# Kernel tuning notes

Hardware: AMD Instinct MI355X
Metric: run time of the kernel (lower is better)

Reference implementation:

```python
import jax, jax.numpy as jnp
import numpy as np

N = 100000   # nodes
E = 400000   # edges per relation
D = 256      # in_dim == out_dim
H = 8        # heads
DK = D // H  # 32
R = 2        # relations
SQRT_DK = float(np.sqrt(DK))


def setup_inputs() -> dict:
    key = jax.random.key(0)
    ks = jax.random.split(key, 16)
    s = 1.0 / np.sqrt(D)
    h = jax.random.normal(ks[0], (N, D), jnp.float32)
    src0 = jax.random.randint(ks[1], (E,), 0, N, jnp.int32)
    dst0 = jax.random.randint(ks[2], (E,), 0, N, jnp.int32)
    src1 = jax.random.randint(ks[3], (E,), 0, N, jnp.int32)
    dst1 = jax.random.randint(ks[4], (E,), 0, N, jnp.int32)
    Wk = jax.random.normal(ks[5], (D, D), jnp.float32) * s
    Wq = jax.random.normal(ks[6], (D, D), jnp.float32) * s
    Wv = jax.random.normal(ks[7], (D, D), jnp.float32) * s
    Wa = jax.random.normal(ks[8], (D, D), jnp.float32) * s
    bk = jnp.zeros((D,), jnp.float32)
    bq = jnp.zeros((D,), jnp.float32)
    bv = jnp.zeros((D,), jnp.float32)
    ba = jnp.zeros((D,), jnp.float32)
    ln_g = jnp.ones((D,), jnp.float32)
    ln_b = jnp.zeros((D,), jnp.float32)
    rel_pri = jnp.ones((R, H), jnp.float32)
    xav = float(np.sqrt(6.0 / (DK + DK)))  # xavier_uniform gain=1
    rel_att = jax.random.uniform(ks[9], (R, H, DK, DK), jnp.float32, -xav, xav)
    rel_msg = jax.random.uniform(ks[10], (R, H, DK, DK), jnp.float32, -xav, xav)
    return dict(h=h, src0=src0, dst0=dst0, src1=src1, dst1=dst1,
                Wk=Wk, bk=bk, Wq=Wq, bq=bq, Wv=Wv, bv=bv, Wa=Wa, ba=ba,
                ln_g=ln_g, ln_b=ln_b, rel_pri=rel_pri, rel_att=rel_att, rel_msg=rel_msg)


def _layernorm(x, g, b):
    m = jnp.mean(x, axis=-1, keepdims=True)
    v = jnp.mean(jnp.square(x - m), axis=-1, keepdims=True)
    return (x - m) * jax.lax.rsqrt(v + 1e-5) * g + b


def reference(h, src0, dst0, src1, dst1, Wk, bk, Wq, bq, Wv, bv, Wa, ba,
              ln_g, ln_b, rel_pri, rel_att, rel_msg):
    # per-type K/Q/V projections -> [N, H, DK]
    k = (h @ Wk + bk).reshape(N, H, DK)
    q = (h @ Wq + bq).reshape(N, H, DK)
    v = (h @ Wv + bv).reshape(N, H, DK)

    def rel_agg(r, src, dst):
        # per-relation transform (einsum 'bij,ijk->bik' in the original)
        kr = jnp.einsum('nhd,hde->nhe', k, rel_att[r])
        vr = jnp.einsum('nhd,hde->nhe', v, rel_msg[r])
        # v_dot_u: per-edge per-head dot product, scaled by relation_pri / sqrt(d_k)
        score = jnp.einsum('ehd,ehd->eh', q[dst], kr[src]) * rel_pri[r] / SQRT_DK  # [E, H]
        # edge_softmax normalized over incoming edges of each dst node
        m = jax.ops.segment_max(score, dst, num_segments=N)
        m = jnp.where(jnp.isfinite(m), m, 0.0)  # empty segments
        ex = jnp.exp(score - m[dst])
        den = jax.ops.segment_sum(ex, dst, num_segments=N)
        attn = ex / den[dst]  # [E, H]
        # u_mul_e + sum aggregation
        msg = vr[src] * attn[:, :, None]  # [E, H, DK]
        return jax.ops.segment_sum(msg, dst, num_segments=N)  # [N, H, DK]

    # cross_reducer='mean' over the two relations
    t = (rel_agg(0, src0, dst0) + rel_agg(1, src1, dst1)) * 0.5
    t = t.reshape(N, D)
    # output projection + residual + LayerNorm (dropout off / eval)
    out = _layernorm(t @ Wa + ba + h, ln_g, ln_b)
    return out
```

## Files before the change

### kernel.cpp

```cpp
#include <hip/hip_runtime.h>
#include <cstdint>
#include <cstddef>


#define NN 100000
#define EE 400000

static constexpr float INV_SQRT_DK = 0.17677669529663687f;

static constexpr size_t OFF_Q      = 0;
static constexpr size_t OFF_KV     = OFF_Q + (size_t)NN * 256;
static constexpr size_t OFF_UNION  = OFF_KV + (size_t)NN * 512;
static constexpr size_t OFF_BBUF   = OFF_UNION;
static constexpr size_t OFF_ROWPTR = OFF_UNION;
static constexpr size_t OFF_CURSOR = OFF_ROWPTR + NN;
static constexpr size_t OFF_SRCS   = OFF_CURSOR + NN;
static constexpr size_t OFF_BIAS   = OFF_UNION + 600000;
static constexpr size_t OFF_BT     = OFF_BIAS + 1280;
static constexpr size_t OFF_END    = OFF_BT + (size_t)1536 * 512 / 2;

using bf16x8 = __attribute__((ext_vector_type(8))) __bf16;
using f32x4v = __attribute__((ext_vector_type(4))) float;
using u32x4  = __attribute__((ext_vector_type(4))) unsigned int;

static __device__ inline unsigned int bf_bits(__bf16 b) {
    union { __bf16 b; unsigned short u; } x; x.b = b; return (unsigned int)x.u;
}
static __device__ inline float bf2f(unsigned short u) {
    union { unsigned int u; float f; } x; x.u = ((unsigned int)u) << 16; return x.f;
}

__global__ __launch_bounds__(256)
void zero_kernel(float4* __restrict__ p, long n4)
{
    const long stride = (long)gridDim.x * blockDim.x;
    for (long i = (long)blockIdx.x * blockDim.x + threadIdx.x; i < n4; i += stride)
        p[i] = make_float4(0.f, 0.f, 0.f, 0.f);
}

__global__ __launch_bounds__(256)
void build_B_kernel(const float* __restrict__ Wk, const float* __restrict__ Wq,
                    const float* __restrict__ Wv,
                    const float* __restrict__ bk, const float* __restrict__ bq,
                    const float* __restrict__ bv,
                    const float* __restrict__ rel_att, const float* __restrict__ rel_msg,
                    float* __restrict__ Bbuf, float* __restrict__ biasbuf)
{
    const int din = blockIdx.x;
    const int t   = threadIdx.x;
    __shared__ float wk[256], wv[256];
    wk[t] = Wk[din * 256 + t];
    wv[t] = Wv[din * 256 + t];
    __syncthreads();
    const int h = t >> 5, e = t & 31;
    Bbuf[(size_t)din * 1280 + t] = Wq[din * 256 + t];
    #pragma unroll
    for (int r = 0; r < 2; ++r) {
        const float* ra = rel_att + (size_t)((r * 8 + h) * 32) * 32 + e;
        const float* rm = rel_msg + (size_t)((r * 8 + h) * 32) * 32 + e;
        float sa = 0.f, sm = 0.f;
        #pragma unroll
        for (int dd = 0; dd < 32; ++dd) {
            sa = fmaf(wk[h * 32 + dd], ra[dd * 32], sa);
            sm = fmaf(wv[h * 32 + dd], rm[dd * 32], sm);
        }
        Bbuf[(size_t)din * 1280 + 256 + r * 512 + t]       = sa;
        Bbuf[(size_t)din * 1280 + 256 + r * 512 + 256 + t] = sm;
    }
    if (din == 0) {
        biasbuf[t] = bq[t];
        #pragma unroll
        for (int r = 0; r < 2; ++r) {
            float sa = 0.f, sm = 0.f;
            #pragma unroll
            for (int dd = 0; dd < 32; ++dd) {
                sa = fmaf(bk[h * 32 + dd], rel_att[(size_t)((r * 8 + h) * 32 + dd) * 32 + e], sa);
                sm = fmaf(bv[h * 32 + dd], rel_msg[(size_t)((r * 8 + h) * 32 + dd) * 32 + e], sm);
            }
            biasbuf[256 + r * 512 + t]       = sa;
            biasbuf[256 + r * 512 + 256 + t] = sm;
        }
    }
}

__global__ __launch_bounds__(256)
void conv_B_kernel(const float* __restrict__ Bbuf, const float* __restrict__ Wa,
                   unsigned short* __restrict__ BT)
{
    const int n = blockIdx.x;
    const int k = threadIdx.x;
    const float v = (n < 1280) ? Bbuf[(size_t)k * 1280 + n]
                               : Wa[(size_t)k * 256 + (n - 1280)];
    __bf16 hi = (__bf16)v;
    __bf16 lo = (__bf16)(v - (float)hi);
    BT[(size_t)n * 512 + k]       = (unsigned short)bf_bits(hi);
    BT[(size_t)n * 512 + 256 + k] = (unsigned short)bf_bits(lo);
}

__global__ __launch_bounds__(256)
void gemm_mfma(const float* __restrict__ A, int lda,
               const unsigned short* __restrict__ BT,
               const float* __restrict__ bias,
               float* __restrict__ Qout, unsigned short* __restrict__ KVout,
               int M, float alpha)
{
    __shared__ __align__(16) unsigned short AsB[128 * 64];
    __shared__ __align__(16) unsigned short BsB[128 * 64];
    const int tid = threadIdx.x;
    const int bn = blockIdx.x * 128;
    const int bm = blockIdx.y * 128;
    const int wid = tid >> 6;
    const int l   = tid & 63;
    const int wm  = (wid >> 1) * 64;
    const int wn  = (wid & 1) * 64;
    const int l15 = l & 15;
    const int k8  = (l >> 4) * 8;

    f32x4v acc[4][4];
    #pragma unroll
    for (int i = 0; i < 4; ++i)
        #pragma unroll
        for (int j = 0; j < 4; ++j)
            acc[i][j] = (f32x4v){0.f, 0.f, 0.f, 0.f};

    float4 rA[2][2];
    u32x4  rB[4];

    auto g_load = [&](int kb) {
        #pragma unroll
        for (int it = 0; it < 2; ++it) {
            const int s = it * 256 + tid;
            const int row = s >> 2, c8 = (s & 3) * 8;
            const float* base = A + (size_t)(bm + row) * lda + kb * 32 + c8;
            const bool ok = (bm + row) < M;
            rA[it][0] = ok ? *reinterpret_cast<const float4*>(base)     : make_float4(0,0,0,0);
            rA[it][1] = ok ? *reinterpret_cast<const float4*>(base + 4) : make_float4(0,0,0,0);
        }
        #pragma unroll
        for (int it = 0; it < 4; ++it) {
            const int s = it * 256 + tid;
            const int row = s >> 3, q = s & 7;
            const char* src = reinterpret_cast<const char*>(BT) + (size_t)(bn + row) * 1024
                              + ((q < 4) ? (kb * 64 + q * 16) : (512 + kb * 64 + (q - 4) * 16));
            rB[it] = *reinterpret_cast<const u32x4*>(src);
        }
    };

    g_load(0);

    for (int kb = 0; kb < 8; ++kb) {
        __syncthreads();
        #pragma unroll
        for (int it = 0; it < 2; ++it) {
            const int s = it * 256 + tid;
            const int row = s >> 2, c8 = (s & 3) * 8;
            float vv[8] = {rA[it][0].x, rA[it][0].y, rA[it][0].z, rA[it][0].w,
                           rA[it][1].x, rA[it][1].y, rA[it][1].z, rA[it][1].w};
            unsigned int hw[4], lw[4];
            #pragma unroll
            for (int j = 0; j < 4; ++j) {
                const __bf16 h0 = (__bf16)vv[2*j],  h1 = (__bf16)vv[2*j+1];
                const float  r0 = vv[2*j] - (float)h0, r1 = vv[2*j+1] - (float)h1;
                const __bf16 l0 = (__bf16)r0, l1 = (__bf16)r1;
                hw[j] = bf_bits(h0) | (bf_bits(h1) << 16);
                lw[j] = bf_bits(l0) | (bf_bits(l1) << 16);
            }
            const int swz = (row & 7) << 4;
            char* basep = reinterpret_cast<char*>(AsB);
            *reinterpret_cast<u32x4*>(basep + ((row * 128 +      c8 * 2) ^ swz)) = (u32x4){hw[0],hw[1],hw[2],hw[3]};
            *reinterpret_cast<u32x4*>(basep + ((row * 128 + 64 + c8 * 2) ^ swz)) = (u32x4){lw[0],lw[1],lw[2],lw[3]};
        }
        #pragma unroll
        for (int it = 0; it < 4; ++it) {
            const int s = it * 256 + tid;
            const int row = s >> 3, q = s & 7;
            const int swz = (row & 7) << 4;
            *reinterpret_cast<u32x4*>(reinterpret_cast<char*>(BsB) + ((row * 128 + q * 16) ^ swz)) = rB[it];
        }
        __syncthreads();
        if (kb < 7) g_load(kb + 1);

        #pragma unroll
        for (int term = 0; term < 3; ++term) {
            const int apart = (term == 1) ? 64 : 0;
            const int bpart = (term == 2) ? 64 : 0;
            bf16x8 af[4], bfr[4];
            #pragma unroll
            for (int i = 0; i < 4; ++i) {
                const int arow = wm + i * 16 + l15;
                af[i]  = *reinterpret_cast<const bf16x8*>(reinterpret_cast<const char*>(AsB)
                           + ((arow * 128 + apart + k8 * 2) ^ ((arow & 7) << 4)));
                const int brow = wn + i * 16 + l15;
                bfr[i] = *reinterpret_cast<const bf16x8*>(reinterpret_cast<const char*>(BsB)
                           + ((brow * 128 + bpart + k8 * 2) ^ ((brow & 7) << 4)));
            }
            #pragma unroll
            for (int i = 0; i < 4; ++i)
                #pragma unroll
                for (int j = 0; j < 4; ++j)
                    acc[i][j] = __builtin_amdgcn_mfma_f32_16x16x32_bf16(af[i], bfr[j], acc[i][j], 0, 0, 0);
        }
    }

    const bool q_seg = (bn < 256);
    #pragma unroll
    for (int i = 0; i < 4; ++i) {
        const int rbase = bm + wm + i * 16 + (l >> 4) * 4;
        #pragma unroll
        for (int j = 0; j < 4; ++j) {
            const int col = bn + wn + j * 16 + l15;
            const float bcol = bias[col];
            #pragma unroll
            for (int r = 0; r < 4; ++r) {
                const int row = rbase + r;
                if (row < M) {
                    const float o = alpha * acc[i][j][r] + bcol;
                    if (q_seg)
                        Qout[(size_t)row * 256 + col] = o;
                    else
                        KVout[(size_t)row * 1024 + (col - 256)] = (unsigned short)bf_bits((__bf16)o);
                }
            }
        }
    }
}

__global__ __launch_bounds__(256)
void hist_kernel(const int* __restrict__ dst, int* __restrict__ deg, int E)
{
    const int stride = gridDim.x * blockDim.x;
    for (int e = blockIdx.x * blockDim.x + threadIdx.x; e < E; e += stride)
        atomicAdd(&deg[dst[e]], 1);
}

__global__ __launch_bounds__(1024)
void scan1_kernel(const int* __restrict__ deg, int* __restrict__ rowptr,
                  int* __restrict__ part, int n)
{
    __shared__ int sm[1024];
    const int tid = threadIdx.x;
    const int i = blockIdx.x * 1024 + tid;
    const int v = (i < n) ? deg[i] : 0;
    sm[tid] = v;
    __syncthreads();
    for (int off = 1; off < 1024; off <<= 1) {
        int add = (tid >= off) ? sm[tid - off] : 0;
        __syncthreads();
        sm[tid] += add;
        __syncthreads();
    }
    if (i < n) rowptr[i] = sm[tid] - v;
    if (tid == 1023) part[blockIdx.x] = sm[1023];
}

__global__ __launch_bounds__(1024)
void scan2_kernel(int* __restrict__ part, int np)
{
    __shared__ int sm[1024];
    const int tid = threadIdx.x;
    const int v = (tid < np) ? part[tid] : 0;
    sm[tid] = v;
    __syncthreads();
    for (int off = 1; off < 1024; off <<= 1) {
        int add = (tid >= off) ? sm[tid - off] : 0;
        __syncthreads();
        sm[tid] += add;
        __syncthreads();
    }
    if (tid < np) part[tid] = sm[tid] - v;
}

__global__ __launch_bounds__(256)
void scan3_kernel(int* __restrict__ rowptr, int* __restrict__ cursor,
                  const int* __restrict__ part, int n)
{
    const int i = blockIdx.x * 256 + threadIdx.x;
    if (i < n) {
        const int r = rowptr[i] + part[i >> 10];
        rowptr[i] = r;
        cursor[i] = r;
    }
}

__global__ __launch_bounds__(256)
void scatter_kernel(const int* __restrict__ src, const int* __restrict__ dst,
                    int* __restrict__ cursor, int* __restrict__ srcs, int E)
{
    const int stride = gridDim.x * blockDim.x;
    for (int e = blockIdx.x * blockDim.x + threadIdx.x; e < E; e += stride) {
        int pos = atomicAdd(&cursor[dst[e]], 1);
        srcs[pos] = src[e];
    }
}

__global__ __launch_bounds__(256)
void node_agg_kernel(const float* __restrict__ Q, const unsigned short* __restrict__ KV,
                     int roff,
                     const int* __restrict__ rowptr, const int* __restrict__ endptr,
                     const int* __restrict__ srcs,
                     const float* __restrict__ pri8,
                     float* __restrict__ AGG, int accumulate)
{
    const int node = (blockIdx.x * blockDim.x + threadIdx.x) >> 6;
    if (node >= NN) return;
    const int l = threadIdx.x & 63;
    const int h = l >> 3;
    const float4 q4 = reinterpret_cast<const float4*>(Q + (size_t)node * 256)[l];
    const float prh = pri8[h] * INV_SQRT_DK;
    const int s0 = rowptr[node];
    const int s1 = endptr[node];
    float m = -3.0e38f, den = 0.f;
    float4 acc = make_float4(0.f, 0.f, 0.f, 0.f);
    for (int i = s0; i < s1; ++i) {
        const int s = srcs[i];
        const unsigned short* kvrow = KV + (size_t)s * 1024 + roff;
        const ushort4 k4 = *reinterpret_cast<const ushort4*>(kvrow + l * 4);
        float p = q4.x * bf2f(k4.x) + q4.y * bf2f(k4.y) + q4.z * bf2f(k4.z) + q4.w * bf2f(k4.w);
        p += __shfl_xor(p, 1, 64);
        p += __shfl_xor(p, 2, 64);
        p += __shfl_xor(p, 4, 64);
        const float sc = p * prh;
        const float mnew = fmaxf(m, sc);
        const float scale = __expf(m - mnew);
        const float ex = __expf(sc - mnew);
        const ushort4 v4 = *reinterpret_cast<const ushort4*>(kvrow + 256 + l * 4);
        den = den * scale + ex;
        acc.x = acc.x * scale + bf2f(v4.x) * ex;
        acc.y = acc.y * scale + bf2f(v4.y) * ex;
        acc.z = acc.z * scale + bf2f(v4.z) * ex;
        acc.w = acc.w * scale + bf2f(v4.w) * ex;
        m = mnew;
    }
    const float inv = (s1 > s0) ? 1.0f / den : 0.f;
    float4 o = make_float4(acc.x * inv, acc.y * inv, acc.z * inv, acc.w * inv);
    float4* outp = reinterpret_cast<float4*>(AGG + (size_t)node * 256);
    if (accumulate) {
        const float4 prev = outp[l];
        o.x += prev.x; o.y += prev.y; o.z += prev.z; o.w += prev.w;
    }
    outp[l] = o;
}

__global__ __launch_bounds__(256)
void ln_kernel(const float* __restrict__ tmp, const float* __restrict__ hres,
               const float* __restrict__ g, const float* __restrict__ b,
               float* __restrict__ out, int M)
{
    const int gtid = blockIdx.x * blockDim.x + threadIdx.x;
    const int wid = gtid >> 6;
    const int nw = (gridDim.x * blockDim.x) >> 6;
    const int lane = threadIdx.x & 63;
    const float4 gv = reinterpret_cast<const float4*>(g)[lane];
    const float4 bv = reinterpret_cast<const float4*>(b)[lane];
    for (int row = wid; row < M; row += nw) {
        const float4 tv = reinterpret_cast<const float4*>(tmp + (size_t)row * 256)[lane];
        const float4 hv = reinterpret_cast<const float4*>(hres + (size_t)row * 256)[lane];
        float y0 = tv.x + hv.x, y1 = tv.y + hv.y, y2 = tv.z + hv.z, y3 = tv.w + hv.w;
        float ssum = y0 + y1 + y2 + y3;
        #pragma unroll
        for (int off = 32; off; off >>= 1) ssum += __shfl_xor(ssum, off, 64);
        const float mean = ssum * (1.f / 256.f);
        const float d0 = y0 - mean, d1 = y1 - mean, d2 = y2 - mean, d3 = y3 - mean;
        float sq = d0 * d0 + d1 * d1 + d2 * d2 + d3 * d3;
        #pragma unroll
        for (int off = 32; off; off >>= 1) sq += __shfl_xor(sq, off, 64);
        const float inv = rsqrtf(sq * (1.f / 256.f) + 1e-5f);
        float4 o;
        o.x = d0 * inv * gv.x + bv.x;
        o.y = d1 * inv * gv.y + bv.y;
        o.z = d2 * inv * gv.z + bv.z;
        o.w = d3 * inv * gv.w + bv.w;
        reinterpret_cast<float4*>(out + (size_t)row * 256)[lane] = o;
    }
}

extern "C" void kernel_launch(void* const* d_in, const int* in_sizes, int n_in,
                              void* d_out, int out_size, void* d_ws, size_t ws_size,
                              hipStream_t stream)
{
    const float* h    = (const float*)d_in[0];
    const int* src0   = (const int*)d_in[1];
    const int* dst0   = (const int*)d_in[2];
    const int* src1   = (const int*)d_in[3];
    const int* dst1   = (const int*)d_in[4];
    const float* Wk   = (const float*)d_in[5];
    const float* bk   = (const float*)d_in[6];
    const float* Wq   = (const float*)d_in[7];
    const float* bq   = (const float*)d_in[8];
    const float* Wv   = (const float*)d_in[9];
    const float* bv   = (const float*)d_in[10];
    const float* Wa   = (const float*)d_in[11];
    const float* ba   = (const float*)d_in[12];
    const float* lng  = (const float*)d_in[13];
    const float* lnb  = (const float*)d_in[14];
    const float* rel_pri = (const float*)d_in[15];
    const float* rel_att = (const float*)d_in[16];
    const float* rel_msg = (const float*)d_in[17];

    float* ws    = (float*)d_ws;
    float* Q     = ws + OFF_Q;
    unsigned short* KV = (unsigned short*)(ws + OFF_KV);
    float* BBUF  = ws + OFF_BBUF;
    float* BIAS  = ws + OFF_BIAS;
    int* ROWPTR  = (int*)(ws + OFF_ROWPTR);
    int* CURSOR  = (int*)(ws + OFF_CURSOR);
    int* SRCS    = (int*)(ws + OFF_SRCS);
    int* PART    = SRCS;
    unsigned short* BT = (unsigned short*)(ws + OFF_BT);
    float* AGG   = (float*)d_out;
    float* TMP   = ws + OFF_Q;

    const int NSCAN = (NN + 1023) / 1024;

    build_B_kernel<<<256, 256, 0, stream>>>(Wk, Wq, Wv, bk, bq, bv,
                                            rel_att, rel_msg, BBUF, BIAS);
    conv_B_kernel<<<1536, 256, 0, stream>>>(BBUF, Wa, BT);

    {
        dim3 grid(1280 / 128, (NN + 127) / 128);
        gemm_mfma<<<grid, 256, 0, stream>>>(h, 256, BT, BIAS, Q, KV, NN, 1.0f);
    }

    zero_kernel<<<128, 256, 0, stream>>>((float4*)CURSOR, (long)NN / 4);
    hist_kernel<<<1024, 256, 0, stream>>>(dst0, CURSOR, EE);
    scan1_kernel<<<NSCAN, 1024, 0, stream>>>(CURSOR, ROWPTR, PART, NN);
    scan2_kernel<<<1, 1024, 0, stream>>>(PART, NSCAN);
    scan3_kernel<<<(NN + 255) / 256, 256, 0, stream>>>(ROWPTR, CURSOR, PART, NN);
    scatter_kernel<<<1024, 256, 0, stream>>>(src0, dst0, CURSOR, SRCS, EE);
    node_agg_kernel<<<NN * 64 / 256, 256, 0, stream>>>(Q, KV, 0, ROWPTR, CURSOR, SRCS,
                                                       rel_pri + 0, AGG, 0);

    zero_kernel<<<128, 256, 0, stream>>>((float4*)CURSOR, (long)NN / 4);
    hist_kernel<<<1024, 256, 0, stream>>>(dst1, CURSOR, EE);
    scan1_kernel<<<NSCAN, 1024, 0, stream>>>(CURSOR, ROWPTR, PART, NN);
    scan2_kernel<<<1, 1024, 0, stream>>>(PART, NSCAN);
    scan3_kernel<<<(NN + 255) / 256, 256, 0, stream>>>(ROWPTR, CURSOR, PART, NN);
    scatter_kernel<<<1024, 256, 0, stream>>>(src1, dst1, CURSOR, SRCS, EE);
    node_agg_kernel<<<NN * 64 / 256, 256, 0, stream>>>(Q, KV, 512, ROWPTR, CURSOR, SRCS,
                                                       rel_pri + 8, AGG, 1);

    {
        dim3 grid(256 / 128, (NN + 127) / 128);
        gemm_mfma<<<grid, 256, 0, stream>>>(AGG, 256, BT + (size_t)1280 * 512, ba,
                                            TMP, KV, NN, 0.5f);
    }
    ln_kernel<<<2048, 256, 0, stream>>>(TMP, h, lng, lnb, (float*)d_out, NN);
}
```

Before: 1.075 ms.

## Merge both relations into one CSR and aggregation pass; async-load B tiles

After: 1.063 ms. About the same (-1.1%).

```diff
diff --git a/kernel.cpp b/kernel.cpp
--- a/kernel.cpp
+++ b/kernel.cpp
@@ -15,7 +15,7 @@
 static constexpr size_t OFF_ROWPTR = OFF_UNION;
 static constexpr size_t OFF_CURSOR = OFF_ROWPTR + NN;
 static constexpr size_t OFF_SRCS   = OFF_CURSOR + NN;
-static constexpr size_t OFF_BIAS   = OFF_UNION + 600000;
+static constexpr size_t OFF_BIAS   = OFF_UNION + 1000000;
 static constexpr size_t OFF_BT     = OFF_BIAS + 1280;
 static constexpr size_t OFF_END    = OFF_BT + (size_t)1536 * 512 / 2;
 
@@ -29,6 +29,10 @@
 static __device__ inline float bf2f(unsigned short u) {
     union { unsigned int u; float f; } x; x.u = ((unsigned int)u) << 16; return x.f;
 }
+
+#define GLOAD_LDS16(gsrc, ldst) \
+    __builtin_amdgcn_global_load_lds((const __attribute__((address_space(1))) void*)(gsrc), \
+                                     (__attribute__((address_space(3))) void*)(ldst), 16, 0, 0)
 
 __global__ __launch_bounds__(256)
 void zero_kernel(float4* __restrict__ p, long n4)
@@ -105,7 +109,7 @@
                int M, float alpha)
 {
     __shared__ __align__(16) unsigned short AsB[128 * 64];
-    __shared__ __align__(16) unsigned short BsB[128 * 64];
+    __shared__ __align__(16) unsigned short BsB[2][128 * 64];
     const int tid = threadIdx.x;
     const int bn = blockIdx.x * 128;
     const int bm = blockIdx.y * 128;
@@ -124,9 +128,8 @@
             acc[i][j] = (f32x4v){0.f, 0.f, 0.f, 0.f};
 
     float4 rA[2][2];
-    u32x4  rB[4];
-
-    auto g_load = [&](int kb) {
+
+    auto g_load_A = [&](int kb) {
         #pragma unroll
         for (int it = 0; it < 2; ++it) {
             const int s = it * 256 + tid;
@@ -136,17 +139,22 @@
             rA[it][0] = ok ? *reinterpret_cast<const float4*>(base)     : make_float4(0,0,0,0);
             rA[it][1] = ok ? *reinterpret_cast<const float4*>(base + 4) : make_float4(0,0,0,0);
         }
+    };
+    auto stage_B = [&](int kb, int buf) {
+        char* lbase = reinterpret_cast<char*>(&BsB[buf][0]);
         #pragma unroll
         for (int it = 0; it < 4; ++it) {
             const int s = it * 256 + tid;
             const int row = s >> 3, q = s & 7;
-            const char* src = reinterpret_cast<const char*>(BT) + (size_t)(bn + row) * 1024
-                              + ((q < 4) ? (kb * 64 + q * 16) : (512 + kb * 64 + (q - 4) * 16));
-            rB[it] = *reinterpret_cast<const u32x4*>(src);
+            const int qq = q ^ (row & 7);
+            const char* gsrc = reinterpret_cast<const char*>(BT) + (size_t)(bn + row) * 1024
+                               + ((qq < 4) ? (kb * 64 + qq * 16) : (512 + kb * 64 + (qq - 4) * 16));
+            GLOAD_LDS16(gsrc, lbase + s * 16);
         }
     };
 
-    g_load(0);
+    stage_B(0, 0);
+    g_load_A(0);
 
     for (int kb = 0; kb < 8; ++kb) {
         __syncthreads();
@@ -170,16 +178,10 @@
             *reinterpret_cast<u32x4*>(basep + ((row * 128 +      c8 * 2) ^ swz)) = (u32x4){hw[0],hw[1],hw[2],hw[3]};
             *reinterpret_cast<u32x4*>(basep + ((row * 128 + 64 + c8 * 2) ^ swz)) = (u32x4){lw[0],lw[1],lw[2],lw[3]};
         }
-        #pragma unroll
-        for (int it = 0; it < 4; ++it) {
-            const int s = it * 256 + tid;
-            const int row = s >> 3, q = s & 7;
-            const int swz = (row & 7) << 4;
-            *reinterpret_cast<u32x4*>(reinterpret_cast<char*>(BsB) + ((row * 128 + q * 16) ^ swz)) = rB[it];
-        }
-        __syncthreads();
-        if (kb < 7) g_load(kb + 1);
-
+        __syncthreads();
+        if (kb < 7) { stage_B(kb + 1, (kb + 1) & 1); g_load_A(kb + 1); }
+
+        const char* bbase = reinterpret_cast<const char*>(&BsB[kb & 1][0]);
         #pragma unroll
         for (int term = 0; term < 3; ++term) {
             const int apart = (term == 1) ? 64 : 0;
@@ -191,7 +193,7 @@
                 af[i]  = *reinterpret_cast<const bf16x8*>(reinterpret_cast<const char*>(AsB)
                            + ((arow * 128 + apart + k8 * 2) ^ ((arow & 7) << 4)));
                 const int brow = wn + i * 16 + l15;
-                bfr[i] = *reinterpret_cast<const bf16x8*>(reinterpret_cast<const char*>(BsB)
+                bfr[i] = *reinterpret_cast<const bf16x8*>(bbase
                            + ((brow * 128 + bpart + k8 * 2) ^ ((brow & 7) << 4)));
             }
             #pragma unroll
@@ -226,11 +228,14 @@
 }
 
 __global__ __launch_bounds__(256)
-void hist_kernel(const int* __restrict__ dst, int* __restrict__ deg, int E)
+void hist2_kernel(const int* __restrict__ dst0, const int* __restrict__ dst1,
+                  int* __restrict__ deg)
 {
     const int stride = gridDim.x * blockDim.x;
-    for (int e = blockIdx.x * blockDim.x + threadIdx.x; e < E; e += stride)
-        atomicAdd(&deg[dst[e]], 1);
+    for (int i = blockIdx.x * blockDim.x + threadIdx.x; i < 2 * EE; i += stride) {
+        const int d = (i < EE) ? dst0[i] : dst1[i - EE];
+        atomicAdd(&deg[d], 1);
+    }
 }
 
 __global__ __launch_bounds__(1024)
@@ -283,62 +288,84 @@
 }
 
 __global__ __launch_bounds__(256)
-void scatter_kernel(const int* __restrict__ src, const int* __restrict__ dst,
-                    int* __restrict__ cursor, int* __restrict__ srcs, int E)
+void scatter2_kernel(const int* __restrict__ src0, const int* __restrict__ dst0,
+                     const int* __restrict__ src1, const int* __restrict__ dst1,
+                     int* __restrict__ cursor, int* __restrict__ srcs)
 {
     const int stride = gridDim.x * blockDim.x;
-    for (int e = blockIdx.x * blockDim.x + threadIdx.x; e < E; e += stride) {
-        int pos = atomicAdd(&cursor[dst[e]], 1);
-        srcs[pos] = src[e];
-    }
-}
-
-__global__ __launch_bounds__(256)
-void node_agg_kernel(const float* __restrict__ Q, const unsigned short* __restrict__ KV,
-                     int roff,
-                     const int* __restrict__ rowptr, const int* __restrict__ endptr,
-                     const int* __restrict__ srcs,
-                     const float* __restrict__ pri8,
-                     float* __restrict__ AGG, int accumulate)
+    for (int i = blockIdx.x * blockDim.x + threadIdx.x; i < 2 * EE; i += stride) {
+        const int rel = (i >= EE);
+        const int e = rel ? (i - EE) : i;
+        const int d  = rel ? dst1[e] : dst0[e];
+        const int sv = (rel ? src1[e] : src0[e]) | (rel << 20);
+        int pos = atomicAdd(&cursor[d], 1);
+        srcs[pos] = sv;
+    }
+}
+
+__global__ __launch_bounds__(256)
+void node_agg2_kernel(const float* __restrict__ Q, const unsigned short* __restrict__ KV,
+                      const int* __restrict__ rowptr, const int* __restrict__ endptr,
+                      const int* __restrict__ srcs,
+                      const float* __restrict__ rel_pri,
+                      float* __restrict__ AGG)
 {
     const int node = (blockIdx.x * blockDim.x + threadIdx.x) >> 6;
     if (node >= NN) return;
     const int l = threadIdx.x & 63;
     const int h = l >> 3;
     const float4 q4 = reinterpret_cast<const float4*>(Q + (size_t)node * 256)[l];
-    const float prh = pri8[h] * INV_SQRT_DK;
+    const float pr0 = rel_pri[h] * INV_SQRT_DK;
+    const float pr1 = rel_pri[8 + h] * INV_SQRT_DK;
     const int s0 = rowptr[node];
     const int s1 = endptr[node];
-    float m = -3.0e38f, den = 0.f;
-    float4 acc = make_float4(0.f, 0.f, 0.f, 0.f);
+    float m0 = -3.0e38f, m1 = -3.0e38f, den0 = 0.f, den1 = 0.f;
+    float4 a0 = make_float4(0.f, 0.f, 0.f, 0.f);
+    float4 a1 = make_float4(0.f, 0.f, 0.f, 0.f);
     for (int i = s0; i < s1; ++i) {
-        const int s = srcs[i];
-        const unsigned short* kvrow = KV + (size_t)s * 1024 + roff;
-        const ushort4 k4 = *reinterpret_cast<const ushort4*>(kvrow + l * 4);
-        float p = q4.x * bf2f(k4.x) + q4.y * bf2f(k4.y) + q4.z * bf2f(k4.z) + q4.w * bf2f(k4.w);
-        p += __shfl_xor(p, 1, 64);
-        p += __shfl_xor(p, 2, 64);
-        p += __shfl_xor(p, 4, 64);
-        const float sc = p * prh;
-        const float mnew = fmaxf(m, sc);
-        const float scale = __expf(m - mnew);
-        const float ex = __expf(sc - mnew);
-        const ushort4 v4 = *reinterpret_cast<const ushort4*>(kvrow + 256 + l * 4);
-        den = den * scale + ex;
-        acc.x = acc.x * scale + bf2f(v4.x) * ex;
-        acc.y = acc.y * scale + bf2f(v4.y) * ex;
-        acc.z = acc.z * scale + bf2f(v4.z) * ex;
-        acc.w = acc.w * scale + bf2f(v4.w) * ex;
-        m = mnew;
-    }
-    const float inv = (s1 > s0) ? 1.0f / den : 0.f;
-    float4 o = make_float4(acc.x * inv, acc.y * inv, acc.z * inv, acc.w * inv);
-    float4* outp = reinterpret_cast<float4*>(AGG + (size_t)node * 256);
-    if (accumulate) {
-        const float4 prev = outp[l];
-        o.x += prev.x; o.y += prev.y; o.z += prev.z; o.w += prev.w;
-    }
-    outp[l] = o;
+        const int p = srcs[i];
+        const int s = p & 0xFFFFF;
+        const int rel = p >> 20;
+        const unsigned short* kv = KV + (size_t)s * 1024 + (rel << 9);
+        const ushort4 k4 = *reinterpret_cast<const ushort4*>(kv + l * 4);
+        float t = q4.x * bf2f(k4.x) + q4.y * bf2f(k4.y) + q4.z * bf2f(k4.z) + q4.w * bf2f(k4.w);
+        t += __shfl_xor(t, 1, 64);
+        t += __shfl_xor(t, 2, 64);
+        t += __shfl_xor(t, 4, 64);
+        const ushort4 v4 = *reinterpret_cast<const ushort4*>(kv + 256 + l * 4);
+        const float vx = bf2f(v4.x), vy = bf2f(v4.y), vz = bf2f(v4.z), vw = bf2f(v4.w);
+        if (rel == 0) {
+            const float sc = t * pr0;
+            const float mn = fmaxf(m0, sc);
+            const float scale = __expf(m0 - mn);
+            const float ex = __expf(sc - mn);
+            den0 = den0 * scale + ex;
+            a0.x = a0.x * scale + vx * ex;
+            a0.y = a0.y * scale + vy * ex;
+            a0.z = a0.z * scale + vz * ex;
+            a0.w = a0.w * scale + vw * ex;
+            m0 = mn;
+        } else {
+            const float sc = t * pr1;
+            const float mn = fmaxf(m1, sc);
+            const float scale = __expf(m1 - mn);
+            const float ex = __expf(sc - mn);
+            den1 = den1 * scale + ex;
+            a1.x = a1.x * scale + vx * ex;
+            a1.y = a1.y * scale + vy * ex;
+            a1.z = a1.z * scale + vz * ex;
+            a1.w = a1.w * scale + vw * ex;
+            m1 = mn;
+        }
+    }
+    const float i0 = (den0 > 0.f) ? 1.0f / den0 : 0.f;
+    const float i1 = (den1 > 0.f) ? 1.0f / den1 : 0.f;
+    float4 o;
+    o.x = a0.x * i0 + a1.x * i1;
+    o.y = a0.y * i0 + a1.y * i1;
+    o.z = a0.z * i0 + a1.z * i1;
+    o.w = a0.w * i0 + a1.w * i1;
+    reinterpret_cast<float4*>(AGG + (size_t)node * 256)[l] = o;
 }
 
 __global__ __launch_bounds__(256)
@@ -422,22 +449,14 @@
     }
 
     zero_kernel<<<128, 256, 0, stream>>>((float4*)CURSOR, (long)NN / 4);
-    hist_kernel<<<1024, 256, 0, stream>>>(dst0, CURSOR, EE);
+    hist2_kernel<<<1024, 256, 0, stream>>>(dst0, dst1, CURSOR);
     scan1_kernel<<<NSCAN, 1024, 0, stream>>>(CURSOR, ROWPTR, PART, NN);
     scan2_kernel<<<1, 1024, 0, stream>>>(PART, NSCAN);
     scan3_kernel<<<(NN + 255) / 256, 256, 0, stream>>>(ROWPTR, CURSOR, PART, NN);
-    scatter_kernel<<<1024, 256, 0, stream>>>(src0, dst0, CURSOR, SRCS, EE);
-    node_agg_kernel<<<NN * 64 / 256, 256, 0, stream>>>(Q, KV, 0, ROWPTR, CURSOR, SRCS,
-                                                       rel_pri + 0, AGG, 0);
-
-    zero_kernel<<<128, 256, 0, stream>>>((float4*)CURSOR, (long)NN / 4);
-    hist_kernel<<<1024, 256, 0, stream>>>(dst1, CURSOR, EE);
-    scan1_kernel<<<NSCAN, 1024, 0, stream>>>(CURSOR, ROWPTR, PART, NN);
-    scan2_kernel<<<1, 1024, 0, stream>>>(PART, NSCAN);
-    scan3_kernel<<<(NN + 255) / 256, 256, 0, stream>>>(ROWPTR, CURSOR, PART, NN);
-    scatter_kernel<<<1024, 256, 0, stream>>>(src1, dst1, CURSOR, SRCS, EE);
-    node_agg_kernel<<<NN * 64 / 256, 256, 0, stream>>>(Q, KV, 512, ROWPTR, CURSOR, SRCS,
-                                                       rel_pri + 8, AGG, 1);
+    scatter2_kernel<<<1024, 256, 0, stream>>>(src0, dst0, src1, dst1, CURSOR, SRCS);
+
+    node_agg2_kernel<<<NN * 64 / 256, 256, 0, stream>>>(Q, KV, ROWPTR, CURSOR, SRCS,
+                                                        rel_pri, AGG);
 
     {
         dim3 grid(256 / 128, (NN + 127) / 128);
```
